# Optimization experiments

Measured on AMD Instinct MI355X. Metric: run time of the kernel, lower is better.

The kernel has to match this reference:

```python
import jax, jax.numpy as jnp
import numpy as np

ALPHA = 0.95   # membrane decay
VTH = 1.0      # firing threshold
BN_EPS = 1e-5
SS_BETA = 10.0  # SuperSpike surrogate slope (used in bwd module)


def _spike(v):
    # Heaviside spike on (v - vth) already subtracted
    return (v > 0).astype(v.dtype)


def _batchnorm(h, scale, bias):
    # per-timestep batch norm over the batch axis (train mode, batch stats)
    mu = jnp.mean(h, axis=0, keepdims=True)
    var = jnp.mean(jnp.square(h - mu), axis=0, keepdims=True)
    return (h - mu) * jax.lax.rsqrt(var + BN_EPS) * scale + bias


def _lif_layer(x, W, scale=None, bias=None):
    # x: [T, B, F_in] -> spikes z: [T, B, F_out]
    T, B, _ = x.shape
    F_out = W.shape[1]
    I = jnp.einsum('tbf,fo->tbo', x, W)  # precompute dense projection for all steps

    def step(v, i_t):
        if scale is not None:
            i_t = _batchnorm(i_t, scale, bias)
        v = ALPHA * v + i_t
        z = _spike(v - VTH)
        v = v * (1.0 - z)  # reset-to-zero
        return v, z

    v0 = jnp.zeros((B, F_out), dtype=x.dtype)
    _, z = jax.lax.scan(step, v0, I)
    return z


def setup_inputs() -> dict:
    key = jax.random.key(0)
    k1, k2, k3 = jax.random.split(key, 3)
    B, T, H, Wd, C = 512, 100, 28, 28, 2
    inputs = jax.random.uniform(k1, (B, T, H, Wd, C), dtype=jnp.float32)
    trgt = jax.random.randint(k2, (B,), 0, 10)
    W1 = jax.random.normal(k3, (784, 100), dtype=jnp.float32) * (1.0 / np.sqrt(784))
    bn_scale = jnp.ones((100,), dtype=jnp.float32)
    bn_bias = jnp.zeros((100,), dtype=jnp.float32)
    W2 = jax.random.normal(jax.random.fold_in(key, 7), (100, 10), dtype=jnp.float32) * (1.0 / np.sqrt(100))
    return {"inputs": inputs, "trgt": trgt, "W1": W1, "bn_scale": bn_scale,
            "bn_bias": bn_bias, "W2": W2}


def reference(inputs, trgt, W1, bn_scale, bn_bias, W2):
    # inputs: [B, T, H, W, C]
    x = jnp.mean(inputs, axis=-1, keepdims=True)        # [B,T,H,W,1]
    x = jnp.swapaxes(x, 0, 1)                            # [T,B,H,W,1]
    x = jnp.reshape(x, (x.shape[0], x.shape[1], -1))     # [T,B,784]
    z1 = _lif_layer(x, W1, bn_scale, bn_bias)            # [T,B,100]
    z2 = _lif_layer(z1, W2)                              # [T,B,10]
    out = jnp.mean(z2, axis=0)                           # [B,10]
    return out
```

## Files before the change

kernel.cpp:

```cpp
#include <hip/hip_runtime.h>

#define T_STEPS 100
#define BATCH   512
#define FIN     784
#define O1      100
#define O2      10
#define KC1     28
#define NC1     (FIN / KC1)

typedef __attribute__((ext_vector_type(4))) double f64x4;

__device__ __forceinline__ void block_sync_lds() {
  __builtin_amdgcn_sched_barrier(0);
  asm volatile("s_waitcnt lgkmcnt(0)" ::: "memory");
  __builtin_amdgcn_s_barrier();
  __builtin_amdgcn_sched_barrier(0);
}

__global__ __launch_bounds__(256) void k1_mfma(const float* __restrict__ in,
                                               const float* __restrict__ W1,
                                               double* __restrict__ I1T) {
  __shared__ double AI[KC1][69];
  const int tid = threadIdx.x;
  const int l   = tid & 63;
  const int w   = tid >> 6;
  const int r16 = l & 15;
  const int q16 = l >> 4;
  const int b0  = (int)blockIdx.x * 64;
  const int t   = (int)blockIdx.y;

  bool iact[4]; int irow[4], iq[4]; const float* ibp[4];
#pragma unroll
  for (int p = 0; p < 4; ++p) {
    const int i = p * 256 + tid;
    iact[p] = (i < 896);
    const int row = iact[p] ? i / 14 : 0;
    iq[p]   = (iact[p] ? i : 0) - row * 14;
    irow[p] = row;
    ibp[p]  = in + ((size_t)(b0 + row) * T_STEPS + t) * (FIN * 2) + iq[p] * 4;
  }

  float4 ist[4];
#pragma unroll
  for (int p = 0; p < 4; ++p) if (iact[p]) ist[p] = *reinterpret_cast<const float4*>(ibp[p]);

  const f64x4 z = {0.0, 0.0, 0.0, 0.0};
  f64x4 pr = __builtin_amdgcn_mfma_f64_16x16x4f64((double)r16, 0.25, z, 0, 0, 0);
  f64x4 pc = __builtin_amdgcn_mfma_f64_16x16x4f64(0.25, (double)r16, z, 0, 0, 0);
  int soff0, soff1, soff2, soff3;
  {
    int rm0 = (int)(pr[0] + 0.5), cm0 = (int)(pc[0] + 0.5);
    int rm1 = (int)(pr[1] + 0.5), cm1 = (int)(pc[1] + 0.5);
    int rm2 = (int)(pr[2] + 0.5), cm2 = (int)(pc[2] + 0.5);
    int rm3 = (int)(pr[3] + 0.5), cm3 = (int)(pc[3] + 0.5);
    soff0 = rm0 * BATCH + cm0; soff1 = rm1 * BATCH + cm1;
    soff2 = rm2 * BATCH + cm2; soff3 = rm3 * BATCH + cm3;
  }

  f64x4 A0 = z, A1 = z, A2 = z, A3 = z, A4 = z, A5 = z, A6 = z;

  const float* pW0 = W1 + (size_t)q16 * O1 + r16;

  for (int c = 0; c < NC1; ++c) {
    block_sync_lds();
    float wreg[7][7];
    const float* pWc = pW0 + (size_t)c * (KC1 * O1);
#pragma unroll
    for (int q = 0; q < 7; ++q) {
      wreg[q][0] = pWc[q * 400 +  0];
      wreg[q][1] = pWc[q * 400 + 16];
      wreg[q][2] = pWc[q * 400 + 32];
      wreg[q][3] = pWc[q * 400 + 48];
      wreg[q][4] = pWc[q * 400 + 64];
      wreg[q][5] = pWc[q * 400 + 80];
      wreg[q][6] = pWc[q * 400 + 84];
    }
#pragma unroll
    for (int p = 0; p < 4; ++p)
      if (iact[p]) {
        AI[iq[p] * 2 + 0][irow[p]] = 0.5 * ((double)ist[p].x + (double)ist[p].y);
        AI[iq[p] * 2 + 1][irow[p]] = 0.5 * ((double)ist[p].z + (double)ist[p].w);
      }
    if (c + 1 < NC1) {
#pragma unroll
      for (int p = 0; p < 4; ++p)
        if (iact[p]) ist[p] = *reinterpret_cast<const float4*>(ibp[p] + (c + 1) * 56);
    }
    block_sync_lds();
#define MFMA_(D, A, B) D = __builtin_amdgcn_mfma_f64_16x16x4f64((A), (B), (D), 0, 0, 0)
#pragma unroll
    for (int q = 0; q < 7; ++q) {
      const double bv = AI[q * 4 + q16][w * 16 + r16];
      MFMA_(A0, (double)wreg[q][0], bv);
      MFMA_(A1, (double)wreg[q][1], bv);
      MFMA_(A2, (double)wreg[q][2], bv);
      MFMA_(A3, (double)wreg[q][3], bv);
      MFMA_(A4, (double)wreg[q][4], bv);
      MFMA_(A5, (double)wreg[q][5], bv);
      MFMA_(A6, (double)wreg[q][6], bv);
    }
#undef MFMA_
  }

  double* base = I1T + ((size_t)t * O1) * BATCH + (b0 + w * 16);
#define ST(ACC, O0)                                                        \
  {                                                                        \
    base[(size_t)(O0) * BATCH + soff0] = (ACC)[0];                         \
    base[(size_t)(O0) * BATCH + soff1] = (ACC)[1];                         \
    base[(size_t)(O0) * BATCH + soff2] = (ACC)[2];                         \
    base[(size_t)(O0) * BATCH + soff3] = (ACC)[3];                         \
  }
  ST(A0, 0); ST(A1, 16); ST(A2, 32); ST(A3, 48);
  ST(A4, 64); ST(A5, 80); ST(A6, 84);
#undef ST
}

__global__ __launch_bounds__(256) void k2_bnstats(const double* __restrict__ I1T,
                                                  double* __restrict__ mu,
                                                  double* __restrict__ rstd) {
  const int r    = blockIdx.x * 4 + (threadIdx.x >> 6);
  const int lane = threadIdx.x & 63;
  const double2* row2 = reinterpret_cast<const double2*>(I1T + (size_t)r * BATCH) + lane * 4;
  double v[8];
#pragma unroll
  for (int u = 0; u < 4; ++u) {
    double2 p = row2[u];
    v[2 * u] = p.x; v[2 * u + 1] = p.y;
  }
  double s = 0.0;
#pragma unroll
  for (int u = 0; u < 8; ++u) s += v[u];
#pragma unroll
  for (int m = 32; m >= 1; m >>= 1) s += __shfl_xor(s, m, 64);
  const double mean = s / 512.0;
  double q = 0.0;
#pragma unroll
  for (int u = 0; u < 8; ++u) { double d = v[u] - mean; q += d * d; }
#pragma unroll
  for (int m = 32; m >= 1; m >>= 1) q += __shfl_xor(q, m, 64);
  if (lane == 0) {
    mu[r]   = mean;
    rstd[r] = 1.0 / sqrt(q / 512.0 + 1e-5);
  }
}

__global__ __launch_bounds__(512) void k3_lif1(const double* __restrict__ I1T,
                                               const double* __restrict__ mu,
                                               const double* __restrict__ rstd,
                                               const float* __restrict__ scale,
                                               const float* __restrict__ bias,
                                               float* __restrict__ z1T) {
  const int o = blockIdx.x;
  const int b = threadIdx.x;
  const double sc = (double)scale[o], bs = (double)bias[o];
  double v = 0.0;
  for (int tc = 0; tc < T_STEPS; tc += 10) {
    double x[10], muv[10], rsv[10];
#pragma unroll
    for (int u = 0; u < 10; ++u) {
      const int t = tc + u;
      x[u]   = I1T[((size_t)t * O1 + o) * BATCH + b];
      muv[u] = mu[t * O1 + o];
      rsv[u] = rstd[t * O1 + o];
    }
#pragma unroll
    for (int u = 0; u < 10; ++u) {
      const double i = ((x[u] - muv[u]) * rsv[u]) * sc + bs;
      v = 0.95 * v + i;
      const bool z = (v > 1.0);
      z1T[((size_t)(tc + u) * O1 + o) * BATCH + b] = z ? 1.0f : 0.0f;
      if (z) v = 0.0;
    }
  }
}

__global__ __launch_bounds__(512) void k4_proj2(const float* __restrict__ z1T,
                                                const float* __restrict__ W2,
                                                double* __restrict__ I2) {
  __shared__ double W2_lds[O1 * O2];
  const int t = blockIdx.x;
  const int b = threadIdx.x;
  for (int i = threadIdx.x; i < O1 * O2; i += 512) W2_lds[i] = (double)W2[i];
  __syncthreads();
  double acc[O2];
#pragma unroll
  for (int j = 0; j < O2; ++j) acc[j] = 0.0;
  for (int o = 0; o < O1; ++o) {
    const double z = (double)z1T[((size_t)t * O1 + o) * BATCH + b];
#pragma unroll
    for (int j = 0; j < O2; ++j) acc[j] += z * W2_lds[o * O2 + j];
  }
#pragma unroll
  for (int j = 0; j < O2; ++j)
    I2[((size_t)t * O2 + j) * BATCH + b] = acc[j];
}

__global__ __launch_bounds__(512) void k5_lif2(const double* __restrict__ I2,
                                               float* __restrict__ out) {
  const int j = blockIdx.x;
  const int b = threadIdx.x;
  double v = 0.0;
  int cnt = 0;
  for (int tc = 0; tc < T_STEPS; tc += 10) {
    double x[10];
#pragma unroll
    for (int u = 0; u < 10; ++u)
      x[u] = I2[((size_t)(tc + u) * O2 + j) * BATCH + b];
#pragma unroll
    for (int u = 0; u < 10; ++u) {
      v = 0.95 * v + x[u];
      if (v > 1.0) { ++cnt; v = 0.0; }
    }
  }
  out[b * O2 + j] = (float)((double)cnt / 100.0);
}

extern "C" void kernel_launch(void* const* d_in, const int* in_sizes, int n_in,
                              void* d_out, int out_size, void* d_ws, size_t ws_size,
                              hipStream_t stream) {
  const float* in    = (const float*)d_in[0];
  const float* W1    = (const float*)d_in[2];
  const float* scale = (const float*)d_in[3];
  const float* bias  = (const float*)d_in[4];
  const float* W2    = (const float*)d_in[5];
  float* out = (float*)d_out;

  char* ws = (char*)d_ws;
  size_t off = 0;
  double* I1T  = (double*)(ws + off); off += (size_t)T_STEPS * O1 * BATCH * sizeof(double);
  double* mu   = (double*)(ws + off); off += (size_t)T_STEPS * O1 * sizeof(double);
  double* rstd = (double*)(ws + off); off += (size_t)T_STEPS * O1 * sizeof(double);
  float*  z1T  = (float*)(ws + off);  off += (size_t)T_STEPS * O1 * BATCH * sizeof(float);
  double* I2   = (double*)(ws + off); off += (size_t)T_STEPS * O2 * BATCH * sizeof(double);

  k1_mfma   <<<dim3(BATCH / 64, T_STEPS), 256, 0, stream>>>(in, W1, I1T);
  k2_bnstats<<<dim3(T_STEPS * O1 / 4), 256, 0, stream>>>(I1T, mu, rstd);
  k3_lif1   <<<dim3(O1), 512, 0, stream>>>(I1T, mu, rstd, scale, bias, z1T);
  k4_proj2  <<<dim3(T_STEPS), 512, 0, stream>>>(z1T, W2, I2);
  k5_lif2   <<<dim3(O2), 512, 0, stream>>>(I2, out);
}
```

Baseline: 288.9 us.

## Load input operands directly into registers, dropping LDS staging and barriers

The first projection kernel no longer stages the channel-averaged input tile in shared memory. Each lane now loads its own float2 pair straight from global memory and computes the channel mean in registers. The K loop is unrolled by two chunks with double-buffered input registers to overlap loads with MFMA work. This removes LDS writes, reads and block barriers, but each wave now issues strided, less coalesced global loads (one float2 per lane, rows far apart) and uses more registers.

```diff
diff --git a/kernel.cpp b/kernel.cpp
--- a/kernel.cpp
+++ b/kernel.cpp
@@ -5,44 +5,19 @@
 #define FIN     784
 #define O1      100
 #define O2      10
-#define KC1     28
-#define NC1     (FIN / KC1)
 
 typedef __attribute__((ext_vector_type(4))) double f64x4;
-
-__device__ __forceinline__ void block_sync_lds() {
-  __builtin_amdgcn_sched_barrier(0);
-  asm volatile("s_waitcnt lgkmcnt(0)" ::: "memory");
-  __builtin_amdgcn_s_barrier();
-  __builtin_amdgcn_sched_barrier(0);
-}
 
 __global__ __launch_bounds__(256) void k1_mfma(const float* __restrict__ in,
                                                const float* __restrict__ W1,
                                                double* __restrict__ I1T) {
-  __shared__ double AI[KC1][69];
   const int tid = threadIdx.x;
   const int l   = tid & 63;
   const int w   = tid >> 6;
   const int r16 = l & 15;
   const int q16 = l >> 4;
-  const int b0  = (int)blockIdx.x * 64;
+  const int b0  = (int)blockIdx.x * 64 + w * 16;
   const int t   = (int)blockIdx.y;
-
-  bool iact[4]; int irow[4], iq[4]; const float* ibp[4];
-#pragma unroll
-  for (int p = 0; p < 4; ++p) {
-    const int i = p * 256 + tid;
-    iact[p] = (i < 896);
-    const int row = iact[p] ? i / 14 : 0;
-    iq[p]   = (iact[p] ? i : 0) - row * 14;
-    irow[p] = row;
-    ibp[p]  = in + ((size_t)(b0 + row) * T_STEPS + t) * (FIN * 2) + iq[p] * 4;
-  }
-
-  float4 ist[4];
-#pragma unroll
-  for (int p = 0; p < 4; ++p) if (iact[p]) ist[p] = *reinterpret_cast<const float4*>(ibp[p]);
 
   const f64x4 z = {0.0, 0.0, 0.0, 0.0};
   f64x4 pr = __builtin_amdgcn_mfma_f64_16x16x4f64((double)r16, 0.25, z, 0, 0, 0);
@@ -57,52 +32,55 @@
     soff2 = rm2 * BATCH + cm2; soff3 = rm3 * BATCH + cm3;
   }
 
+  const float2* pB = reinterpret_cast<const float2*>(in) +
+                     ((size_t)(b0 + r16) * T_STEPS + t) * FIN + q16;
+  const float* pW = W1 + (size_t)q16 * O1 + r16;
+
   f64x4 A0 = z, A1 = z, A2 = z, A3 = z, A4 = z, A5 = z, A6 = z;
 
-  const float* pW0 = W1 + (size_t)q16 * O1 + r16;
-
-  for (int c = 0; c < NC1; ++c) {
-    block_sync_lds();
-    float wreg[7][7];
-    const float* pWc = pW0 + (size_t)c * (KC1 * O1);
-#pragma unroll
-    for (int q = 0; q < 7; ++q) {
-      wreg[q][0] = pWc[q * 400 +  0];
-      wreg[q][1] = pWc[q * 400 + 16];
-      wreg[q][2] = pWc[q * 400 + 32];
-      wreg[q][3] = pWc[q * 400 + 48];
-      wreg[q][4] = pWc[q * 400 + 64];
-      wreg[q][5] = pWc[q * 400 + 80];
-      wreg[q][6] = pWc[q * 400 + 84];
-    }
-#pragma unroll
-    for (int p = 0; p < 4; ++p)
-      if (iact[p]) {
-        AI[iq[p] * 2 + 0][irow[p]] = 0.5 * ((double)ist[p].x + (double)ist[p].y);
-        AI[iq[p] * 2 + 1][irow[p]] = 0.5 * ((double)ist[p].z + (double)ist[p].w);
-      }
-    if (c + 1 < NC1) {
-#pragma unroll
-      for (int p = 0; p < 4; ++p)
-        if (iact[p]) ist[p] = *reinterpret_cast<const float4*>(ibp[p] + (c + 1) * 56);
-    }
-    block_sync_lds();
-#define MFMA_(D, A, B) D = __builtin_amdgcn_mfma_f64_16x16x4f64((A), (B), (D), 0, 0, 0)
-#pragma unroll
-    for (int q = 0; q < 7; ++q) {
-      const double bv = AI[q * 4 + q16][w * 16 + r16];
-      MFMA_(A0, (double)wreg[q][0], bv);
-      MFMA_(A1, (double)wreg[q][1], bv);
-      MFMA_(A2, (double)wreg[q][2], bv);
-      MFMA_(A3, (double)wreg[q][3], bv);
-      MFMA_(A4, (double)wreg[q][4], bv);
-      MFMA_(A5, (double)wreg[q][5], bv);
-      MFMA_(A6, (double)wreg[q][6], bv);
-    }
-#undef MFMA_
-  }
-
-  double* base = I1T + ((size_t)t * O1) * BATCH + (b0 + w * 16);
+  float2 Bp[7], Bn[7];
+#pragma unroll
+  for (int q = 0; q < 7; ++q) Bp[q] = pB[4 * q];
+
+#define MF(D, Aop, Bop) D = __builtin_amdgcn_mfma_f64_16x16x4f64((Aop), (Bop), (D), 0, 0, 0)
+#define LOADW(DST, C)                                                     \
+  _Pragma("unroll")                                                       \
+  for (int q = 0; q < 7; ++q) {                                           \
+    const float* pw = pW + (size_t)((C) * 7 + q) * 400;                   \
+    DST[q][0] = pw[0];  DST[q][1] = pw[16]; DST[q][2] = pw[32];           \
+    DST[q][3] = pw[48]; DST[q][4] = pw[64]; DST[q][5] = pw[80];           \
+    DST[q][6] = pw[84];                                                   \
+  }
+#define COMPUTE(BS, WS)                                                   \
+  _Pragma("unroll")                                                       \
+  for (int q = 0; q < 7; ++q) {                                           \
+    const double bv = 0.5 * ((double)BS[q].x + (double)BS[q].y);          \
+    MF(A0, (double)WS[q][0], bv); MF(A1, (double)WS[q][1], bv);           \
+    MF(A2, (double)WS[q][2], bv); MF(A3, (double)WS[q][3], bv);           \
+    MF(A4, (double)WS[q][4], bv); MF(A5, (double)WS[q][5], bv);           \
+    MF(A6, (double)WS[q][6], bv);                                         \
+  }
+
+  for (int cc = 0; cc < 14; ++cc) {
+    const int c0 = 2 * cc, c1 = c0 + 1;
+    float Wa[7][7];
+    LOADW(Wa, c0);
+#pragma unroll
+    for (int q = 0; q < 7; ++q) Bn[q] = pB[(c1 * 7 + q) * 4];
+    COMPUTE(Bp, Wa);
+    float Wb[7][7];
+    LOADW(Wb, c1);
+    if (cc < 13) {
+#pragma unroll
+      for (int q = 0; q < 7; ++q) Bp[q] = pB[((c0 + 2) * 7 + q) * 4];
+    }
+    COMPUTE(Bn, Wb);
+  }
+#undef COMPUTE
+#undef LOADW
+#undef MF
+
+  double* base = I1T + ((size_t)t * O1) * BATCH + b0;
 #define ST(ACC, O0)                                                        \
   {                                                                        \
     base[(size_t)(O0) * BATCH + soff0] = (ACC)[0];                         \
```

Result: slower. 364.7 us (+26.2%).

## Make each wave stage its own input rows in LDS, removing block barriers

Applied to the files above, without the earlier changes.

Each wavefront now loads and converts only its own 16 batch rows into a private double-buffered LDS slice, so the two workgroup barriers per K-chunk are gone. W1 register loads for the next chunk are issued after the current chunk's MFMAs, prefetching them. This aims to cut barrier stalls and hide global load latency, at the cost of more LDS, more live registers, and reliance on wave-level LDS ordering without explicit waits.

```diff
diff --git a/kernel.cpp b/kernel.cpp
--- a/kernel.cpp
+++ b/kernel.cpp
@@ -5,35 +5,27 @@
 #define FIN     784
 #define O1      100
 #define O2      10
-#define KC1     28
-#define NC1     (FIN / KC1)
+#define NC1     28
 
 typedef __attribute__((ext_vector_type(4))) double f64x4;
-
-__device__ __forceinline__ void block_sync_lds() {
-  __builtin_amdgcn_sched_barrier(0);
-  asm volatile("s_waitcnt lgkmcnt(0)" ::: "memory");
-  __builtin_amdgcn_s_barrier();
-  __builtin_amdgcn_sched_barrier(0);
-}
 
 __global__ __launch_bounds__(256) void k1_mfma(const float* __restrict__ in,
                                                const float* __restrict__ W1,
                                                double* __restrict__ I1T) {
-  __shared__ double AI[KC1][69];
+  __shared__ double AI[2][4][NC1][17];
   const int tid = threadIdx.x;
   const int l   = tid & 63;
   const int w   = tid >> 6;
   const int r16 = l & 15;
   const int q16 = l >> 4;
-  const int b0  = (int)blockIdx.x * 64;
+  const int b0  = (int)blockIdx.x * 64 + w * 16;
   const int t   = (int)blockIdx.y;
 
   bool iact[4]; int irow[4], iq[4]; const float* ibp[4];
 #pragma unroll
   for (int p = 0; p < 4; ++p) {
-    const int i = p * 256 + tid;
-    iact[p] = (i < 896);
+    const int i = p * 64 + l;
+    iact[p] = (i < 224);
     const int row = iact[p] ? i / 14 : 0;
     iq[p]   = (iact[p] ? i : 0) - row * 14;
     irow[p] = row;
@@ -57,52 +49,58 @@
     soff2 = rm2 * BATCH + cm2; soff3 = rm3 * BATCH + cm3;
   }
 
+  const float* pW = W1 + (size_t)q16 * O1 + r16;
+
   f64x4 A0 = z, A1 = z, A2 = z, A3 = z, A4 = z, A5 = z, A6 = z;
 
-  const float* pW0 = W1 + (size_t)q16 * O1 + r16;
-
+  float wreg[7][7];
+#pragma unroll
+  for (int q = 0; q < 7; ++q) {
+    const float* pw = pW + (size_t)q * 400;
+    wreg[q][0] = pw[0];  wreg[q][1] = pw[16]; wreg[q][2] = pw[32];
+    wreg[q][3] = pw[48]; wreg[q][4] = pw[64]; wreg[q][5] = pw[80];
+    wreg[q][6] = pw[84];
+  }
+
+#define MF(D, Aop, Bop) D = __builtin_amdgcn_mfma_f64_16x16x4f64((Aop), (Bop), (D), 0, 0, 0)
   for (int c = 0; c < NC1; ++c) {
-    block_sync_lds();
-    float wreg[7][7];
-    const float* pWc = pW0 + (size_t)c * (KC1 * O1);
-#pragma unroll
-    for (int q = 0; q < 7; ++q) {
-      wreg[q][0] = pWc[q * 400 +  0];
-      wreg[q][1] = pWc[q * 400 + 16];
-      wreg[q][2] = pWc[q * 400 + 32];
-      wreg[q][3] = pWc[q * 400 + 48];
-      wreg[q][4] = pWc[q * 400 + 64];
-      wreg[q][5] = pWc[q * 400 + 80];
-      wreg[q][6] = pWc[q * 400 + 84];
-    }
+    const int buf = c & 1;
 #pragma unroll
     for (int p = 0; p < 4; ++p)
       if (iact[p]) {
-        AI[iq[p] * 2 + 0][irow[p]] = 0.5 * ((double)ist[p].x + (double)ist[p].y);
-        AI[iq[p] * 2 + 1][irow[p]] = 0.5 * ((double)ist[p].z + (double)ist[p].w);
+        AI[buf][w][iq[p] * 2 + 0][irow[p]] = 0.5 * ((double)ist[p].x + (double)ist[p].y);
+        AI[buf][w][iq[p] * 2 + 1][irow[p]] = 0.5 * ((double)ist[p].z + (double)ist[p].w);
       }
     if (c + 1 < NC1) {
 #pragma unroll
       for (int p = 0; p < 4; ++p)
         if (iact[p]) ist[p] = *reinterpret_cast<const float4*>(ibp[p] + (c + 1) * 56);
     }
-    block_sync_lds();
-#define MFMA_(D, A, B) D = __builtin_amdgcn_mfma_f64_16x16x4f64((A), (B), (D), 0, 0, 0)
 #pragma unroll
     for (int q = 0; q < 7; ++q) {
-      const double bv = AI[q * 4 + q16][w * 16 + r16];
-      MFMA_(A0, (double)wreg[q][0], bv);
-      MFMA_(A1, (double)wreg[q][1], bv);
-      MFMA_(A2, (double)wreg[q][2], bv);
-      MFMA_(A3, (double)wreg[q][3], bv);
-      MFMA_(A4, (double)wreg[q][4], bv);
-      MFMA_(A5, (double)wreg[q][5], bv);
-      MFMA_(A6, (double)wreg[q][6], bv);
-    }
-#undef MFMA_
-  }
-
-  double* base = I1T + ((size_t)t * O1) * BATCH + (b0 + w * 16);
+      const double bv = AI[buf][w][q * 4 + q16][r16];
+      MF(A0, (double)wreg[q][0], bv);
+      MF(A1, (double)wreg[q][1], bv);
+      MF(A2, (double)wreg[q][2], bv);
+      MF(A3, (double)wreg[q][3], bv);
+      MF(A4, (double)wreg[q][4], bv);
+      MF(A5, (double)wreg[q][5], bv);
+      MF(A6, (double)wreg[q][6], bv);
+    }
+    if (c + 1 < NC1) {
+      const float* pWc = pW + (size_t)(c + 1) * (28 * O1);
+#pragma unroll
+      for (int q = 0; q < 7; ++q) {
+        const float* pw = pWc + (size_t)q * 400;
+        wreg[q][0] = pw[0];  wreg[q][1] = pw[16]; wreg[q][2] = pw[32];
+        wreg[q][3] = pw[48]; wreg[q][4] = pw[64]; wreg[q][5] = pw[80];
+        wreg[q][6] = pw[84];
+      }
+    }
+  }
+#undef MF
+
+  double* base = I1T + ((size_t)t * O1) * BATCH + b0;
 #define ST(ACC, O0)                                                        \
   {                                                                        \
     base[(size_t)(O0) * BATCH + soff0] = (ACC)[0];                         \
```

Measured after the change: 273.2 us. -5.4%, faster.
